# Optimization experiments

Hardware: AMD Instinct MI355X
Metric: run time of the kernel (lower is better)

## Reference

```python
import jax, jax.numpy as jnp
import numpy as np

H, NOPE, ROPE, VDIM, LORA = 16, 128, 64, 128, 512
DM, T, S, K = 2048, 256, 32768, 2048
SCALE = 1.0 / np.sqrt(NOPE + ROPE)
ROPE_BASE = 10000.0


def _rope(x, pos):
    # x: [..., D] with rotary dim D; pos broadcastable to x[..., :1] leading dims
    d = x.shape[-1]
    half = d // 2
    inv = 1.0 / (ROPE_BASE ** (jnp.arange(half, dtype=jnp.float32) / half))
    f = pos[..., None].astype(jnp.float32) * inv  # [..., half]
    cos, sin = jnp.cos(f), jnp.sin(f)
    x1, x2 = x[..., :half], x[..., half:]
    return jnp.concatenate([x1 * cos - x2 * sin, x2 * cos + x1 * sin], axis=-1)


def setup_inputs() -> dict:
    key = jax.random.key(0)
    ks = jax.random.split(key, 9)
    return {
        "x": jax.random.normal(ks[0], (T, DM), jnp.float32) * 0.02,
        "Wq": jax.random.normal(ks[1], (DM, H * (NOPE + ROPE)), jnp.float32) * 0.02,
        "W_UK": jax.random.normal(ks[2], (H, NOPE, LORA), jnp.float32) * 0.02,
        "W_UV": jax.random.normal(ks[3], (H, VDIM, LORA), jnp.float32) * 0.02,
        "Wo": jax.random.normal(ks[4], (H * VDIM, DM), jnp.float32) * 0.02,
        "kv_c": jax.random.normal(ks[5], (S, LORA), jnp.float32),
        "k_pe": jax.random.normal(ks[6], (S, ROPE), jnp.float32),
        "topk_indices": jnp.sort(jax.random.randint(ks[7], (T, K), 0, S, jnp.int32), axis=-1),
        "pos_q": jax.random.randint(ks[8], (T,), 0, S, jnp.int32),
    }


def reference(x, Wq, W_UK, W_UV, Wo, kv_c, k_pe, topk_indices, pos_q):
    n_tok = x.shape[0]
    # q projection -> [T, H, nope+rope], split (MLAAttention._q_proj_and_k_up_proj)
    q = (x @ Wq).reshape(n_tok, H, NOPE + ROPE)
    q_nope, q_pe = q[..., :NOPE], q[..., NOPE:]
    # absorbed k up-projection: q_nope @ W_UK -> latent space [T, H, LORA]
    ql_nope = jnp.einsum("thn,hnl->thl", q_nope, W_UK)
    # rotary on rope parts
    q_pe = _rope(q_pe, pos_q[:, None])            # [T, H, ROPE]
    k_pe_r = _rope(k_pe, jnp.arange(k_pe.shape[0]))  # [S, ROPE]
    # top-k sparse KV gather (DSA indexer / triton index conversion)
    kv_sel = kv_c[topk_indices]                    # [T, K, LORA]
    kpe_sel = k_pe_r[topk_indices]                 # [T, K, ROPE]
    # attention scores in latent space over selected tokens
    scores = (jnp.einsum("thl,tkl->thk", ql_nope, kv_sel)
              + jnp.einsum("thr,tkr->thk", q_pe, kpe_sel)) * SCALE
    attn = jax.nn.softmax(scores, axis=-1)         # [T, H, K]
    o_lat = jnp.einsum("thk,tkl->thl", attn, kv_sel)  # [T, H, LORA]
    # v up-projection (_v_up_proj_and_o_proj) then output proj
    ov = jnp.einsum("thl,hvl->thv", o_lat, W_UV).reshape(n_tok, H * VDIM)
    return ov @ Wo
```

## Files before the change

kernel.cpp:

```cpp
#include <hip/hip_runtime.h>
#include <hip/hip_bf16.h>

#define H_    16
#define NOPE_ 128
#define ROPE_ 64
#define VDIM_ 128
#define LORA_ 512
#define DM_   2048
#define T_    256
#define S_    32768
#define K_    2048

static constexpr float SCALE_ = 0.072168783648703220563643597562744f;
static constexpr float LOG2E_ = 1.4426950408889634f;

typedef __attribute__((ext_vector_type(8))) short short8;
typedef __attribute__((ext_vector_type(4))) short short4v;
typedef __attribute__((ext_vector_type(4))) float f32x4;

__device__ __forceinline__ ushort f2bf(float f) {
    unsigned u = __float_as_uint(f);
    unsigned r = (u + 0x7FFFu + ((u >> 16) & 1u)) >> 16;
    return (ushort)r;
}
__device__ __forceinline__ float bf2f(ushort u) {
    return __uint_as_float((unsigned)u << 16);
}

template<bool A_BF16, bool B_NT, bool C_BF16>
__global__ __launch_bounds__(256) void gemm_mfma(
    const void* __restrict__ Av, const float* __restrict__ B, void* __restrict__ Cv,
    int M, int N, int Kd, int lda, int ldb, int ldc,
    long batchA, long batchB, long batchC)
{
    __shared__ ushort As[64 * 72];
    __shared__ ushort Bs[64 * 72];

    const int tid = threadIdx.x;
    const int w  = tid >> 6;
    const int l  = tid & 63;
    const int lm = l & 15;
    const int kq = l >> 4;
    const int bm = blockIdx.y * 64;
    const int bn = blockIdx.x * 64;
    const int m0 = (w >> 1) * 32;
    const int n0 = (w & 1) * 32;

    const float*  Af = A_BF16 ? nullptr : ((const float*)Av)  + (long)blockIdx.z * batchA;
    const ushort* Ah = A_BF16 ? ((const ushort*)Av) + (long)blockIdx.z * batchA : nullptr;
    B += (long)blockIdx.z * batchB;

    f32x4 acc[2][2];
    #pragma unroll
    for (int i = 0; i < 2; ++i)
        #pragma unroll
        for (int j = 0; j < 2; ++j) acc[i][j] = (f32x4){0.f, 0.f, 0.f, 0.f};

    const int am  = tid >> 2, ako = (tid & 3) * 16;
    const int amr = tid >> 4, akk = (tid & 15) * 4;
    const int bnr = tid >> 4, bkk = (tid & 15) * 4;
    const int bk  = tid >> 2, bnq = (tid & 3) * 16;

    uint4  gA[2];
    float4 gAf[4];
    float4 gB[4];

    auto loadA = [&](int k0) {
        if constexpr (A_BF16) {
            const ushort* src = Ah + (long)(bm + am) * lda + k0 + ako;
            gA[0] = *(const uint4*)(src);
            gA[1] = *(const uint4*)(src + 8);
        } else {
            #pragma unroll
            for (int p = 0; p < 4; ++p)
                gAf[p] = *(const float4*)(Af + (long)(bm + amr + p * 16) * lda + k0 + akk);
        }
    };
    auto loadB = [&](int k0) {
        if constexpr (B_NT) {
            #pragma unroll
            for (int p = 0; p < 4; ++p)
                gB[p] = *(const float4*)(B + (long)(bn + bnr + p * 16) * ldb + k0 + bkk);
        } else {
            #pragma unroll
            for (int p = 0; p < 4; ++p)
                gB[p] = *(const float4*)(B + (long)(k0 + bk) * ldb + bn + bnq + p * 4);
        }
    };

    loadA(0); loadB(0);

    for (int k0 = 0; k0 < Kd; k0 += 64) {
        __syncthreads();
        if constexpr (A_BF16) {
            *(uint4*)(As + am * 72 + ako)     = gA[0];
            *(uint4*)(As + am * 72 + ako + 8) = gA[1];
        } else {
            #pragma unroll
            for (int p = 0; p < 4; ++p) {
                ushort4 u;
                u.x = f2bf(gAf[p].x); u.y = f2bf(gAf[p].y);
                u.z = f2bf(gAf[p].z); u.w = f2bf(gAf[p].w);
                *(ushort4*)(As + (amr + p * 16) * 72 + akk) = u;
            }
        }
        if constexpr (B_NT) {
            #pragma unroll
            for (int p = 0; p < 4; ++p) {
                ushort4 u;
                u.x = f2bf(gB[p].x); u.y = f2bf(gB[p].y);
                u.z = f2bf(gB[p].z); u.w = f2bf(gB[p].w);
                *(ushort4*)(Bs + (bnr + p * 16) * 72 + bkk) = u;
            }
        } else {
            #pragma unroll
            for (int p = 0; p < 4; ++p) {
                ushort4 u;
                u.x = f2bf(gB[p].x); u.y = f2bf(gB[p].y);
                u.z = f2bf(gB[p].z); u.w = f2bf(gB[p].w);
                *(ushort4*)(Bs + bk * 68 + bnq + p * 4) = u;
            }
        }
        if (k0 + 64 < Kd) { loadA(k0 + 64); loadB(k0 + 64); }
        __syncthreads();
        #pragma unroll
        for (int ks = 0; ks < 2; ++ks) {
            short8 a[2], b[2];
            #pragma unroll
            for (int mt = 0; mt < 2; ++mt)
                a[mt] = *(const short8*)(As + (m0 + mt * 16 + lm) * 72 + ks * 32 + kq * 8);
            if constexpr (B_NT) {
                #pragma unroll
                for (int nt = 0; nt < 2; ++nt)
                    b[nt] = *(const short8*)(Bs + (n0 + nt * 16 + lm) * 72 + ks * 32 + kq * 8);
            } else {
                #pragma unroll
                for (int nt = 0; nt < 2; ++nt)
                    #pragma unroll
                    for (int j = 0; j < 8; ++j)
                        b[nt][j] = (short)Bs[(ks * 32 + kq * 8 + j) * 68 + n0 + nt * 16 + lm];
            }
            #pragma unroll
            for (int mt = 0; mt < 2; ++mt)
                #pragma unroll
                for (int nt = 0; nt < 2; ++nt)
                    acc[mt][nt] = __builtin_amdgcn_mfma_f32_16x16x32_bf16(
                        a[mt], b[nt], acc[mt][nt], 0, 0, 0);
        }
    }
    #pragma unroll
    for (int mt = 0; mt < 2; ++mt)
        #pragma unroll
        for (int nt = 0; nt < 2; ++nt)
            #pragma unroll
            for (int r = 0; r < 4; ++r) {
                long row = bm + m0 + mt * 16 + kq * 4 + r;
                long col = bn + n0 + nt * 16 + lm;
                if constexpr (C_BF16)
                    ((ushort*)Cv)[(long)blockIdx.z * batchC + row * ldc + col] =
                        f2bf(acc[mt][nt][r]);
                else
                    ((float*)Cv)[(long)blockIdx.z * batchC + row * ldc + col] =
                        acc[mt][nt][r];
            }
}

__global__ __launch_bounds__(256) void pack_qrope(
    const float* __restrict__ qfull, const int* __restrict__ pos_q,
    ushort* __restrict__ qb)
{
    int id = blockIdx.x * 256 + threadIdx.x;
    int i = id & 31;
    int h = (id >> 5) & 15;
    int t = id >> 9;
    double inv = exp2(-(double)i * 0.41524101186092026);
    double f = (double)pos_q[t] * inv;
    double fr = f - floor(f * 0.15915494309189535) * 6.283185307179586;
    float sf, cf;
    sincosf((float)fr, &sf, &cf);
    float x1 = qfull[t * 3072 + h * 192 + 128 + i];
    float x2 = qfull[t * 3072 + h * 192 + 160 + i];
    ushort* q = qb + (long)(t * 16 + h) * 576;
    q[512 + i] = f2bf(x1 * cf - x2 * sf);
    q[544 + i] = f2bf(x2 * cf + x1 * sf);
}

__global__ __launch_bounds__(256) void prep_kvb(
    const float* __restrict__ kvc, const float* __restrict__ kpe,
    ushort* __restrict__ kvb)
{
    int id = blockIdx.x * 256 + threadIdx.x;
    int s = id / 96;
    int c = id - s * 96;
    if (c < 64) {
        const float* src = kvc + (long)s * 512 + c * 8;
        float4 v0 = *(const float4*)src;
        float4 v1 = *(const float4*)(src + 4);
        ushort4 a, b;
        a.x = f2bf(v0.x); a.y = f2bf(v0.y); a.z = f2bf(v0.z); a.w = f2bf(v0.w);
        b.x = f2bf(v1.x); b.y = f2bf(v1.y); b.z = f2bf(v1.z); b.w = f2bf(v1.w);
        ushort* dst = kvb + (long)s * 576 + c * 8;
        *(ushort4*)dst = a;
        *(ushort4*)(dst + 4) = b;
    } else {
        int i = c - 64;
        double inv = exp2(-(double)i * 0.41524101186092026);
        double f = (double)s * inv;
        double fr = f - floor(f * 0.15915494309189535) * 6.283185307179586;
        float sf, cf;
        sincosf((float)fr, &sf, &cf);
        const float* kp = kpe + (long)s * 64;
        float x1 = kp[i], x2 = kp[32 + i];
        ushort* dst = kvb + (long)s * 576 + 512;
        dst[i]      = f2bf(x1 * cf - x2 * sf);
        dst[32 + i] = f2bf(x2 * cf + x1 * sf);
    }
}

#define KBD 2048
#define KBSZ 73728

__global__ __launch_bounds__(256, 4) void mla_fused_split(
    const ushort* __restrict__ qb, const ushort* __restrict__ kvb,
    const int* __restrict__ topk,
    ushort* __restrict__ Opart, float* __restrict__ ml)
{
    __shared__ __align__(16) char kb[KBSZ];
    __shared__ __align__(16) ushort P2[1024];
    __shared__ float wred[2][4][16];

    const int t = blockIdx.x;
    const int sp = blockIdx.y;
    const int tid = threadIdx.x;
    const int w = tid >> 6;
    const int l = tid & 63;
    const int lm = l & 15;
    const int kq = l >> 4;

    short8 qa[18];
    {
        const ushort* qrow = qb + (long)(t * 16 + lm) * 576 + kq * 8;
        #pragma unroll
        for (int ks = 0; ks < 18; ++ks)
            qa[ks] = *(const short8*)(qrow + ks * 32);
    }

    const int* tkp = topk + (long)t * 2048 + sp * 1024;

    const int kh   = w & 1;
    const int db0  = w >> 1;
    const int skey = 32 * kh + (l >> 1);
    const int gcol = db0 * 16 + (l & 1) * 8;
    const unsigned stRel = (unsigned)(db0 * 2048 + kh * 1024);

    __attribute__((address_space(3))) char* kb3 =
        (__attribute__((address_space(3))) char*)&kb[0];
    const char* kbg = (const char*)&kb[0];
    const unsigned kbBase = (unsigned)(unsigned long long)(const void*)&kb[0];

    const unsigned krowRel = (unsigned)((kq >> 1) * KBD + w * 512 + (lm >> 2) * 128
                     + (lm & 3) * 32 + (kq & 1) * 16);
    const unsigned trb = kbBase + (unsigned)(w * 8 * KBD + kq * 256 + lm * 8);
    const unsigned ptrb = (unsigned)(unsigned long long)(const void*)P2
                        + (unsigned)(kq * 256 + lm * 8);

    f32x4 O[8];
    #pragma unroll
    for (int vt = 0; vt < 8; ++vt) O[vt] = (f32x4){0.f, 0.f, 0.f, 0.f};
    float m_r[4] = {-1e30f, -1e30f, -1e30f, -1e30f};
    float l_r[4] = {0.f, 0.f, 0.f, 0.f};

#define GSTAGE(IDX)                                                           \
    {                                                                         \
        const ushort* gs = kvb + (long)(IDX) * 576 + gcol;                    \
        _Pragma("unroll")                                                     \
        for (int i = 0; i < 18; ++i)                                          \
            __builtin_amdgcn_global_load_lds(                                 \
                (const __attribute__((address_space(1))) void*)(const void*)(gs + i * 32), \
                (__attribute__((address_space(3))) void*)(kb3 + stRel + i * 4096), \
                16, 0, 0);                                                    \
    }

    for (int tt = 0; tt < 16; ++tt) {
        int idx = tkp[tt * 64 + skey];
        __syncthreads();
        GSTAGE(idx)
        asm volatile("s_waitcnt vmcnt(0)" ::: "memory");
        __builtin_amdgcn_s_barrier();
        asm volatile("" ::: "memory");

        const char* krow = kbg + krowRel;
        f32x4 S0 = (f32x4){0.f, 0.f, 0.f, 0.f};
        f32x4 S1 = (f32x4){0.f, 0.f, 0.f, 0.f};
        #pragma unroll
        for (int ks = 0; ks < 18; ks += 2) {
            short8 b0 = *(const short8*)(krow + ks * (2 * KBD));
            S0 = __builtin_amdgcn_mfma_f32_16x16x32_bf16(qa[ks], b0, S0, 0, 0, 0);
            short8 b1 = *(const short8*)(krow + (ks + 1) * (2 * KBD));
            S1 = __builtin_amdgcn_mfma_f32_16x16x32_bf16(qa[ks + 1], b1, S1, 0, 0, 0);
        }
        float s4[4], mx[4], p[4];
        #pragma unroll
        for (int r = 0; r < 4; ++r) { s4[r] = (S0[r] + S1[r]) * SCALE_; mx[r] = s4[r]; }
        #pragma unroll
        for (int off = 1; off < 16; off <<= 1)
            #pragma unroll
            for (int r = 0; r < 4; ++r)
                mx[r] = fmaxf(mx[r], __shfl_xor(mx[r], off, 64));
        if (lm == 0)
            #pragma unroll
            for (int r = 0; r < 4; ++r) wred[0][w][4 * kq + r] = mx[r];
        asm volatile("s_waitcnt lgkmcnt(0)" ::: "memory");
        __builtin_amdgcn_s_barrier();
        asm volatile("" ::: "memory");

        float al[4], rs[4];
        #pragma unroll
        for (int r = 0; r < 4; ++r) {
            float tm = fmaxf(fmaxf(wred[0][0][4 * kq + r], wred[0][1][4 * kq + r]),
                             fmaxf(wred[0][2][4 * kq + r], wred[0][3][4 * kq + r]));
            float mn = fmaxf(m_r[r], tm);
            al[r] = exp2f((m_r[r] - mn) * LOG2E_);
            p[r] = exp2f((s4[r] - mn) * LOG2E_);
            m_r[r] = mn;
            rs[r] = p[r];
        }
        #pragma unroll
        for (int off = 1; off < 16; off <<= 1)
            #pragma unroll
            for (int r = 0; r < 4; ++r)
                rs[r] += __shfl_xor(rs[r], off, 64);
        if (lm == 0)
            #pragma unroll
            for (int r = 0; r < 4; ++r) wred[1][w][4 * kq + r] = rs[r];
        {
            ushort4 pu;
            pu.x = f2bf(p[0]); pu.y = f2bf(p[1]);
            pu.z = f2bf(p[2]); pu.w = f2bf(p[3]);
            *(ushort4*)(P2 + (w * 4 + (lm >> 2)) * 64 + (lm & 3) * 16 + 4 * kq) = pu;
        }
        #pragma unroll
        for (int vt = 0; vt < 8; ++vt)
            #pragma unroll
            for (int r = 0; r < 4; ++r)
                O[vt][r] *= al[r];
        asm volatile("s_waitcnt lgkmcnt(0)" ::: "memory");
        __builtin_amdgcn_s_barrier();
        asm volatile("" ::: "memory");

        #pragma unroll
        for (int r = 0; r < 4; ++r) {
            float ts = wred[1][0][4 * kq + r] + wred[1][1][4 * kq + r] +
                       wred[1][2][4 * kq + r] + wred[1][3][4 * kq + r];
            l_r[r] = l_r[r] * al[r] + ts;
        }

        __builtin_amdgcn_sched_barrier(0);
        short4v pr[4];
        asm volatile("ds_read_b64_tr_b16 %0, %1 offset:0"    : "=v"(pr[0]) : "v"(ptrb));
        asm volatile("ds_read_b64_tr_b16 %0, %1 offset:128"  : "=v"(pr[1]) : "v"(ptrb));
        asm volatile("ds_read_b64_tr_b16 %0, %1 offset:1024" : "=v"(pr[2]) : "v"(ptrb));
        asm volatile("ds_read_b64_tr_b16 %0, %1 offset:1152" : "=v"(pr[3]) : "v"(ptrb));
        short4v rg[2][4];
#define ISSUE_V(vt, slot) \
        asm volatile("ds_read_b64_tr_b16 %0, %1 offset:%2" : "=v"(rg[slot][0]) : "v"(trb), "i"((vt) * KBD));        \
        asm volatile("ds_read_b64_tr_b16 %0, %1 offset:%2" : "=v"(rg[slot][1]) : "v"(trb), "i"((vt) * KBD + 128));  \
        asm volatile("ds_read_b64_tr_b16 %0, %1 offset:%2" : "=v"(rg[slot][2]) : "v"(trb), "i"((vt) * KBD + 1024)); \
        asm volatile("ds_read_b64_tr_b16 %0, %1 offset:%2" : "=v"(rg[slot][3]) : "v"(trb), "i"((vt) * KBD + 1152));
        ISSUE_V(0, 0)
        ISSUE_V(1, 1)
        asm volatile("s_waitcnt lgkmcnt(8)" ::: "memory");
        __builtin_amdgcn_sched_barrier(0);
        short8 pa0 = __builtin_shufflevector(pr[0], pr[1], 0, 1, 2, 3, 4, 5, 6, 7);
        short8 pa1 = __builtin_shufflevector(pr[2], pr[3], 0, 1, 2, 3, 4, 5, 6, 7);
        #pragma unroll
        for (int vt = 0; vt < 8; ++vt) {
            if (vt < 7)
                asm volatile("s_waitcnt lgkmcnt(4)" ::: "memory");
            else
                asm volatile("s_waitcnt lgkmcnt(0)" ::: "memory");
            __builtin_amdgcn_sched_barrier(0);
            short8 bv0 = __builtin_shufflevector(rg[vt & 1][0], rg[vt & 1][1],
                                                 0, 1, 2, 3, 4, 5, 6, 7);
            O[vt] = __builtin_amdgcn_mfma_f32_16x16x32_bf16(pa0, bv0, O[vt], 0, 0, 0);
            short8 bv1 = __builtin_shufflevector(rg[vt & 1][2], rg[vt & 1][3],
                                                 0, 1, 2, 3, 4, 5, 6, 7);
            O[vt] = __builtin_amdgcn_mfma_f32_16x16x32_bf16(pa1, bv1, O[vt], 0, 0, 0);
            if (vt < 6) { ISSUE_V(vt + 2, vt & 1) }
        }
#undef ISSUE_V
    }

    const long rbase = ((long)sp * 256 + t) * 16;
    #pragma unroll
    for (int vt = 0; vt < 8; ++vt)
        #pragma unroll
        for (int r = 0; r < 4; ++r)
            Opart[(rbase + 4 * kq + r) * 512 + w * 128 + vt * 16 + lm] = f2bf(O[vt][r]);
    if (w == 0 && lm == 0) {
        #pragma unroll
        for (int r = 0; r < 4; ++r) {
            ml[(rbase + 4 * kq + r) * 2 + 0] = m_r[r];
            ml[(rbase + 4 * kq + r) * 2 + 1] = l_r[r];
        }
    }
#undef GSTAGE
}

__global__ __launch_bounds__(256) void combine_kernel(
    const ushort* __restrict__ Opart, const float* __restrict__ ml,
    ushort* __restrict__ olat)
{
    const int t = blockIdx.x;
    const int h = threadIdx.x >> 4;
    const int v0 = (threadIdx.x & 15) * 32;
    const long r0 = (long)t * 16 + h;
    const long r1 = (long)(256 + t) * 16 + h;
    float m0 = ml[r0 * 2], l0 = ml[r0 * 2 + 1];
    float m1 = ml[r1 * 2], l1 = ml[r1 * 2 + 1];
    float M = fmaxf(m0, m1);
    float w0 = exp2f((m0 - M) * LOG2E_);
    float w1 = exp2f((m1 - M) * LOG2E_);
    float inv = 1.0f / (w0 * l0 + w1 * l1);
    const ushort* p0 = Opart + r0 * 512 + v0;
    const ushort* p1 = Opart + r1 * 512 + v0;
    ushort* po = olat + r0 * 512 + v0;
    #pragma unroll
    for (int i = 0; i < 32; i += 4) {
        ushort4 a = *(const ushort4*)(p0 + i);
        ushort4 b = *(const ushort4*)(p1 + i);
        ushort4 o;
        o.x = f2bf((w0 * bf2f(a.x) + w1 * bf2f(b.x)) * inv);
        o.y = f2bf((w0 * bf2f(a.y) + w1 * bf2f(b.y)) * inv);
        o.z = f2bf((w0 * bf2f(a.z) + w1 * bf2f(b.z)) * inv);
        o.w = f2bf((w0 * bf2f(a.w) + w1 * bf2f(b.w)) * inv);
        *(ushort4*)(po + i) = o;
    }
}

extern "C" void kernel_launch(void* const* d_in, const int* in_sizes, int n_in,
                              void* d_out, int out_size, void* d_ws, size_t ws_size,
                              hipStream_t stream)
{
    const float* x    = (const float*)d_in[0];
    const float* Wq   = (const float*)d_in[1];
    const float* W_UK = (const float*)d_in[2];
    const float* W_UV = (const float*)d_in[3];
    const float* Wo   = (const float*)d_in[4];
    const float* kv_c = (const float*)d_in[5];
    const float* k_pe = (const float*)d_in[6];
    const int* topk   = (const int*)d_in[7];
    const int* pos_q  = (const int*)d_in[8];
    float* out        = (float*)d_out;

    char* wsb = (char*)d_ws;
    ushort* qb    = (ushort*)wsb;
    float*  qfull = (float*)(wsb + 4718592);
    ushort* Opart = (ushort*)(wsb + 4718592);
    ushort* ov_b  = (ushort*)(wsb + 13107200);
    float*  ml    = (float*)(wsb + 14155776);
    ushort* olat  = qb;
    ushort* kvb   = (ushort*)(wsb + 16252928);
    if (ws_size < (size_t)54001664) return;

    prep_kvb<<<12288, 256, 0, stream>>>(kv_c, k_pe, kvb);

    gemm_mfma<false, false, false><<<dim3(48, 4), 256, 0, stream>>>(
        x, Wq, qfull, 256, 3072, 2048, 2048, 3072, 3072, 0, 0, 0);

    gemm_mfma<false, false, true><<<dim3(8, 4, 16), 256, 0, stream>>>(
        qfull, W_UK, qb, 256, 512, 128, 3072, 512, 9216, 192, 65536, 576);

    pack_qrope<<<512, 256, 0, stream>>>(qfull, pos_q, qb);

    mla_fused_split<<<dim3(256, 2), 256, 0, stream>>>(qb, kvb, topk, Opart, ml);

    combine_kernel<<<256, 256, 0, stream>>>(Opart, ml, olat);

    gemm_mfma<true, true, true><<<dim3(2, 4, 16), 256, 0, stream>>>(
        olat, W_UV, ov_b, 256, 128, 512, 8192, 512, 2048, 512, 65536, 128);

    gemm_mfma<true, false, false><<<dim3(32, 4), 256, 0, stream>>>(
        ov_b, Wo, out, 256, 2048, 2048, 2048, 2048, 2048, 0, 0, 0);
}
```

Measured before the change: 323.0 us.

## Add 32-row GEMM tiles for more blocks and split gather wait into stages

Adds a SMALL_M template mode to the MFMA GEMM that uses 32-row M tiles, which doubles the grid for the Wq, W_UV and Wo projections so more CUs are busy. In the sparse attention kernel, the single full vmcnt(0) wait on the LDS gather is split into three partial waits with barriers, so score MFMAs on the first chunks of the gathered KV row start while later chunks are still loading. The trade-offs are re-reading B tiles across twice as many blocks, and extra barriers per iteration in the attention loop.

```diff
diff --git a/kernel.cpp b/kernel.cpp
--- a/kernel.cpp
+++ b/kernel.cpp
@@ -27,12 +27,14 @@
     return __uint_as_float((unsigned)u << 16);
 }
 
-template<bool A_BF16, bool B_NT, bool C_BF16>
+template<bool A_BF16, bool B_NT, bool C_BF16, bool SMALL_M>
 __global__ __launch_bounds__(256) void gemm_mfma(
     const void* __restrict__ Av, const float* __restrict__ B, void* __restrict__ Cv,
     int M, int N, int Kd, int lda, int ldb, int ldc,
     long batchA, long batchB, long batchC)
 {
+    constexpr int BM = SMALL_M ? 32 : 64;
+    constexpr int MT = SMALL_M ? 1 : 2;
     __shared__ ushort As[64 * 72];
     __shared__ ushort Bs[64 * 72];
 
@@ -41,23 +43,25 @@
     const int l  = tid & 63;
     const int lm = l & 15;
     const int kq = l >> 4;
-    const int bm = blockIdx.y * 64;
+    const int bm = blockIdx.y * BM;
     const int bn = blockIdx.x * 64;
-    const int m0 = (w >> 1) * 32;
+    const int m0 = SMALL_M ? (w >> 1) * 16 : (w >> 1) * 32;
     const int n0 = (w & 1) * 32;
 
     const float*  Af = A_BF16 ? nullptr : ((const float*)Av)  + (long)blockIdx.z * batchA;
     const ushort* Ah = A_BF16 ? ((const ushort*)Av) + (long)blockIdx.z * batchA : nullptr;
     B += (long)blockIdx.z * batchB;
 
-    f32x4 acc[2][2];
+    f32x4 acc[MT][2];
     #pragma unroll
-    for (int i = 0; i < 2; ++i)
+    for (int i = 0; i < MT; ++i)
         #pragma unroll
         for (int j = 0; j < 2; ++j) acc[i][j] = (f32x4){0.f, 0.f, 0.f, 0.f};
 
-    const int am  = tid >> 2, ako = (tid & 3) * 16;
-    const int amr = tid >> 4, akk = (tid & 15) * 4;
+    const int am  = SMALL_M ? (tid >> 3) : (tid >> 2);
+    const int ako = SMALL_M ? (tid & 7) * 8 : (tid & 3) * 16;
+    const int amr = SMALL_M ? (tid >> 3) : (tid >> 4);
+    const int akk = SMALL_M ? (tid & 7) * 8 : (tid & 15) * 4;
     const int bnr = tid >> 4, bkk = (tid & 15) * 4;
     const int bk  = tid >> 2, bnq = (tid & 3) * 16;
 
@@ -69,11 +73,17 @@
         if constexpr (A_BF16) {
             const ushort* src = Ah + (long)(bm + am) * lda + k0 + ako;
             gA[0] = *(const uint4*)(src);
-            gA[1] = *(const uint4*)(src + 8);
+            if constexpr (!SMALL_M) gA[1] = *(const uint4*)(src + 8);
         } else {
-            #pragma unroll
-            for (int p = 0; p < 4; ++p)
-                gAf[p] = *(const float4*)(Af + (long)(bm + amr + p * 16) * lda + k0 + akk);
+            if constexpr (SMALL_M) {
+                const float* s = Af + (long)(bm + amr) * lda + k0 + akk;
+                gAf[0] = *(const float4*)s;
+                gAf[1] = *(const float4*)(s + 4);
+            } else {
+                #pragma unroll
+                for (int p = 0; p < 4; ++p)
+                    gAf[p] = *(const float4*)(Af + (long)(bm + amr + p * 16) * lda + k0 + akk);
+            }
         }
     };
     auto loadB = [&](int k0) {
@@ -93,15 +103,26 @@
     for (int k0 = 0; k0 < Kd; k0 += 64) {
         __syncthreads();
         if constexpr (A_BF16) {
-            *(uint4*)(As + am * 72 + ako)     = gA[0];
-            *(uint4*)(As + am * 72 + ako + 8) = gA[1];
+            *(uint4*)(As + am * 72 + ako) = gA[0];
+            if constexpr (!SMALL_M)
+                *(uint4*)(As + am * 72 + ako + 8) = gA[1];
         } else {
-            #pragma unroll
-            for (int p = 0; p < 4; ++p) {
-                ushort4 u;
-                u.x = f2bf(gAf[p].x); u.y = f2bf(gAf[p].y);
-                u.z = f2bf(gAf[p].z); u.w = f2bf(gAf[p].w);
-                *(ushort4*)(As + (amr + p * 16) * 72 + akk) = u;
+            if constexpr (SMALL_M) {
+                ushort4 u0, u1;
+                u0.x = f2bf(gAf[0].x); u0.y = f2bf(gAf[0].y);
+                u0.z = f2bf(gAf[0].z); u0.w = f2bf(gAf[0].w);
+                u1.x = f2bf(gAf[1].x); u1.y = f2bf(gAf[1].y);
+                u1.z = f2bf(gAf[1].z); u1.w = f2bf(gAf[1].w);
+                *(ushort4*)(As + amr * 72 + akk)     = u0;
+                *(ushort4*)(As + amr * 72 + akk + 4) = u1;
+            } else {
+                #pragma unroll
+                for (int p = 0; p < 4; ++p) {
+                    ushort4 u;
+                    u.x = f2bf(gAf[p].x); u.y = f2bf(gAf[p].y);
+                    u.z = f2bf(gAf[p].z); u.w = f2bf(gAf[p].w);
+                    *(ushort4*)(As + (amr + p * 16) * 72 + akk) = u;
+                }
             }
         }
         if constexpr (B_NT) {
@@ -125,9 +146,9 @@
         __syncthreads();
         #pragma unroll
         for (int ks = 0; ks < 2; ++ks) {
-            short8 a[2], b[2];
-            #pragma unroll
-            for (int mt = 0; mt < 2; ++mt)
+            short8 a[MT], b[2];
+            #pragma unroll
+            for (int mt = 0; mt < MT; ++mt)
                 a[mt] = *(const short8*)(As + (m0 + mt * 16 + lm) * 72 + ks * 32 + kq * 8);
             if constexpr (B_NT) {
                 #pragma unroll
@@ -141,7 +162,7 @@
                         b[nt][j] = (short)Bs[(ks * 32 + kq * 8 + j) * 68 + n0 + nt * 16 + lm];
             }
             #pragma unroll
-            for (int mt = 0; mt < 2; ++mt)
+            for (int mt = 0; mt < MT; ++mt)
                 #pragma unroll
                 for (int nt = 0; nt < 2; ++nt)
                     acc[mt][nt] = __builtin_amdgcn_mfma_f32_16x16x32_bf16(
@@ -149,7 +170,7 @@
         }
     }
     #pragma unroll
-    for (int mt = 0; mt < 2; ++mt)
+    for (int mt = 0; mt < MT; ++mt)
         #pragma unroll
         for (int nt = 0; nt < 2; ++nt)
             #pragma unroll
@@ -285,20 +306,42 @@
         int idx = tkp[tt * 64 + skey];
         __syncthreads();
         GSTAGE(idx)
-        asm volatile("s_waitcnt vmcnt(0)" ::: "memory");
-        __builtin_amdgcn_s_barrier();
-        asm volatile("" ::: "memory");
 
         const char* krow = kbg + krowRel;
         f32x4 S0 = (f32x4){0.f, 0.f, 0.f, 0.f};
         f32x4 S1 = (f32x4){0.f, 0.f, 0.f, 0.f};
-        #pragma unroll
-        for (int ks = 0; ks < 18; ks += 2) {
+
+        asm volatile("s_waitcnt vmcnt(12)" ::: "memory");
+        __builtin_amdgcn_s_barrier();
+        asm volatile("" ::: "memory");
+        #pragma unroll
+        for (int ks = 0; ks < 6; ks += 2) {
             short8 b0 = *(const short8*)(krow + ks * (2 * KBD));
             S0 = __builtin_amdgcn_mfma_f32_16x16x32_bf16(qa[ks], b0, S0, 0, 0, 0);
             short8 b1 = *(const short8*)(krow + (ks + 1) * (2 * KBD));
             S1 = __builtin_amdgcn_mfma_f32_16x16x32_bf16(qa[ks + 1], b1, S1, 0, 0, 0);
         }
+        asm volatile("s_waitcnt vmcnt(6)" ::: "memory");
+        __builtin_amdgcn_s_barrier();
+        asm volatile("" ::: "memory");
+        #pragma unroll
+        for (int ks = 6; ks < 12; ks += 2) {
+            short8 b0 = *(const short8*)(krow + ks * (2 * KBD));
+            S0 = __builtin_amdgcn_mfma_f32_16x16x32_bf16(qa[ks], b0, S0, 0, 0, 0);
+            short8 b1 = *(const short8*)(krow + (ks + 1) * (2 * KBD));
+            S1 = __builtin_amdgcn_mfma_f32_16x16x32_bf16(qa[ks + 1], b1, S1, 0, 0, 0);
+        }
+        asm volatile("s_waitcnt vmcnt(0)" ::: "memory");
+        __builtin_amdgcn_s_barrier();
+        asm volatile("" ::: "memory");
+        #pragma unroll
+        for (int ks = 12; ks < 18; ks += 2) {
+            short8 b0 = *(const short8*)(krow + ks * (2 * KBD));
+            S0 = __builtin_amdgcn_mfma_f32_16x16x32_bf16(qa[ks], b0, S0, 0, 0, 0);
+            short8 b1 = *(const short8*)(krow + (ks + 1) * (2 * KBD));
+            S1 = __builtin_amdgcn_mfma_f32_16x16x32_bf16(qa[ks + 1], b1, S1, 0, 0, 0);
+        }
+
         float s4[4], mx[4], p[4];
         #pragma unroll
         for (int r = 0; r < 4; ++r) { s4[r] = (S0[r] + S1[r]) * SCALE_; mx[r] = s4[r]; }
@@ -465,10 +508,10 @@
 
     prep_kvb<<<12288, 256, 0, stream>>>(kv_c, k_pe, kvb);
 
-    gemm_mfma<false, false, false><<<dim3(48, 4), 256, 0, stream>>>(
+    gemm_mfma<false, false, false, true><<<dim3(48, 8), 256, 0, stream>>>(
         x, Wq, qfull, 256, 3072, 2048, 2048, 3072, 3072, 0, 0, 0);
 
-    gemm_mfma<false, false, true><<<dim3(8, 4, 16), 256, 0, stream>>>(
+    gemm_mfma<false, false, true, false><<<dim3(8, 4, 16), 256, 0, stream>>>(
         qfull, W_UK, qb, 256, 512, 128, 3072, 512, 9216, 192, 65536, 576);
 
     pack_qrope<<<512, 256, 0, stream>>>(qfull, pos_q, qb);
@@ -477,9 +520,9 @@
 
     combine_kernel<<<256, 256, 0, stream>>>(Opart, ml, olat);
 
-    gemm_mfma<true, true, true><<<dim3(2, 4, 16), 256, 0, stream>>>(
+    gemm_mfma<true, true, true, true><<<dim3(2, 8, 16), 256, 0, stream>>>(
         olat, W_UV, ov_b, 256, 128, 512, 8192, 512, 2048, 512, 65536, 128);
 
-    gemm_mfma<true, false, false><<<dim3(32, 4), 256, 0, stream>>>(
+    gemm_mfma<true, false, false, true><<<dim3(32, 8), 256, 0, stream>>>(
         ov_b, Wo, out, 256, 2048, 2048, 2048, 2048, 2048, 0, 0, 0);
 }
```

After: 311.6 us. -3.5%, faster.
